# Kernel tuning notes

Hardware: AMD Instinct MI355X
Metric: run time of the kernel (lower is better)

## Reference

```python
import jax, jax.numpy as jnp
import numpy as np


def setup_inputs() -> dict:
    key = jax.random.key(0)
    k1, k2 = jax.random.split(key)
    query = jax.random.normal(k1, (1, 1024), dtype=jnp.float32)
    keys = jax.random.normal(k2, (32768, 1024), dtype=jnp.float32)
    return {"query": query, "keys": keys}


def reference(query, keys):
    # query: [1, H] -> squeeze to [H]; keys: [S, H]
    q = jnp.squeeze(query)                       # [H]
    dots = keys @ q                              # [S]
    q_norm = jnp.linalg.norm(q)                  # scalar
    k_norms = jnp.linalg.norm(keys, axis=-1)     # [S]
    cos_scores = dots / (q_norm * k_norms)       # [S] cosine similarity per key
    context = jnp.sum(cos_scores[:, None] * keys, axis=0)  # [H]
    return context[None, :]                      # [1, H]
```

## Files before the change

kernel.cpp:

```cpp
#include <hip/hip_runtime.h>


constexpr int H   = 1024;
constexpr int TPB = 256;
constexpr int WPB = TPB / 64;
constexpr int NBLOCKS = 512;
constexpr int R2_CHUNKS = 16;


template <bool USE_WS>
__global__ __launch_bounds__(TPB, 2)
void cosctx_main(const float* __restrict__ q,
                 const float* __restrict__ keys,
                 int S,
                 float* __restrict__ out,
                 float* __restrict__ ws)
{
    const int lane  = threadIdx.x & 63;
    const int wave  = threadIdx.x >> 6;
    const int gwave = blockIdx.x * WPB + wave;
    const int nwaves = gridDim.x * WPB;

    const float4* q4 = reinterpret_cast<const float4*>(q);
    const float4* k4 = reinterpret_cast<const float4*>(keys);

    float4 qv[4];
#pragma unroll
    for (int j = 0; j < 4; ++j) qv[j] = q4[j * 64 + lane];

    float qsq = 0.f;
#pragma unroll
    for (int j = 0; j < 4; ++j)
        qsq += qv[j].x * qv[j].x + qv[j].y * qv[j].y +
               qv[j].z * qv[j].z + qv[j].w * qv[j].w;
#pragma unroll
    for (int off = 32; off > 0; off >>= 1) qsq += __shfl_down(qsq, off, 64);
    const float inv_qn = rsqrtf(__shfl(qsq, 0, 64));

    float4 acc[4];
#pragma unroll
    for (int j = 0; j < 4; ++j) acc[j] = make_float4(0.f, 0.f, 0.f, 0.f);

    int row = gwave;
    float4 kv[4];
    if (row < S) {
        const float4* kr = k4 + (size_t)row * (H / 4);
#pragma unroll
        for (int j = 0; j < 4; ++j) kv[j] = kr[j * 64 + lane];
    }
    while (row < S) {
        const int nrow = row + nwaves;
        float4 kn[4];
        if (nrow < S) {
            const float4* kr = k4 + (size_t)nrow * (H / 4);
#pragma unroll
            for (int j = 0; j < 4; ++j) kn[j] = kr[j * 64 + lane];
        }

        float dot = 0.f, ksq = 0.f;
#pragma unroll
        for (int j = 0; j < 4; ++j) {
            dot += kv[j].x * qv[j].x + kv[j].y * qv[j].y +
                   kv[j].z * qv[j].z + kv[j].w * qv[j].w;
            ksq += kv[j].x * kv[j].x + kv[j].y * kv[j].y +
                   kv[j].z * kv[j].z + kv[j].w * kv[j].w;
        }
#pragma unroll
        for (int off = 32; off > 0; off >>= 1) {
            dot += __shfl_down(dot, off, 64);
            ksq += __shfl_down(ksq, off, 64);
        }
        const float score = __shfl(dot, 0, 64) * inv_qn *
                            rsqrtf(__shfl(ksq, 0, 64));

#pragma unroll
        for (int j = 0; j < 4; ++j) {
            acc[j].x += score * kv[j].x;
            acc[j].y += score * kv[j].y;
            acc[j].z += score * kv[j].z;
            acc[j].w += score * kv[j].w;
        }
#pragma unroll
        for (int j = 0; j < 4; ++j) kv[j] = kn[j];
        row = nrow;
    }

    __shared__ float sacc[WPB][H];
    float4* sa4 = reinterpret_cast<float4*>(sacc[wave]);
#pragma unroll
    for (int j = 0; j < 4; ++j) sa4[j * 64 + lane] = acc[j];
    __syncthreads();

    float4 v = make_float4(0.f, 0.f, 0.f, 0.f);
#pragma unroll
    for (int w = 0; w < WPB; ++w) {
        float4 u = reinterpret_cast<const float4*>(sacc[w])[threadIdx.x];
        v.x += u.x; v.y += u.y; v.z += u.z; v.w += u.w;
    }

    if (USE_WS) {
        reinterpret_cast<float4*>(ws)[(size_t)blockIdx.x * (H / 4) + threadIdx.x] = v;
    } else {
        const int c = threadIdx.x * 4;
        atomicAdd(out + c + 0, v.x);
        atomicAdd(out + c + 1, v.y);
        atomicAdd(out + c + 2, v.z);
        atomicAdd(out + c + 3, v.w);
    }
}

__global__ __launch_bounds__(256)
void cosctx_reduce(const float* __restrict__ ws, float* __restrict__ out)
{
    const int g  = blockIdx.x & 3;
    const int ch = blockIdx.x >> 2;
    const int c  = g * 256 + threadIdx.x;
    const int bpc = NBLOCKS / R2_CHUNKS;
    const int b0 = ch * bpc;
    float s = 0.f;
#pragma unroll 4
    for (int b = b0; b < b0 + bpc; ++b)
        s += ws[(size_t)b * H + c];
    atomicAdd(out + c, s);
}

extern "C" void kernel_launch(void* const* d_in, const int* in_sizes, int n_in,
                              void* d_out, int out_size, void* d_ws, size_t ws_size,
                              hipStream_t stream)
{
    const float* q    = (const float*)d_in[0];
    const float* keys = (const float*)d_in[1];
    float* out        = (float*)d_out;
    const int S = in_sizes[1] / H;

    hipMemsetAsync(out, 0, H * sizeof(float), stream);

    const size_t ws_need = (size_t)NBLOCKS * H * sizeof(float);
    if (ws_size >= ws_need) {
        cosctx_main<true><<<NBLOCKS, TPB, 0, stream>>>(q, keys, S, out, (float*)d_ws);
        cosctx_reduce<<<4 * R2_CHUNKS, 256, 0, stream>>>((const float*)d_ws, out);
    } else {
        cosctx_main<false><<<NBLOCKS, TPB, 0, stream>>>(q, keys, S, out, nullptr);
    }
}
```

Baseline: 195.8 us.

## Process two rows per iteration with deeper prefetch and atomic-free final reduction

The main loop now handles two key rows per iteration and prefetches the next two, which doubles the loads in flight per wave to better hide HBM latency. The second-stage reduction is rewritten so that each block fully reduces a 64-column slice across all partial blocks using float4 loads and shared memory, then writes the output directly. This removes the memset and the atomics on the workspace path. Holding more float4 registers may lower occupancy under launch_bounds(256,2).

```diff
diff --git a/kernel.cpp b/kernel.cpp
--- a/kernel.cpp
+++ b/kernel.cpp
@@ -5,7 +5,7 @@
 constexpr int TPB = 256;
 constexpr int WPB = TPB / 64;
 constexpr int NBLOCKS = 512;
-constexpr int R2_CHUNKS = 16;
+constexpr int RED_BLOCKS = H / 64;
 
 
 template <bool USE_WS>
@@ -19,7 +19,7 @@
     const int lane  = threadIdx.x & 63;
     const int wave  = threadIdx.x >> 6;
     const int gwave = blockIdx.x * WPB + wave;
-    const int nwaves = gridDim.x * WPB;
+    const int nw    = gridDim.x * WPB;
 
     const float4* q4 = reinterpret_cast<const float4*>(q);
     const float4* k4 = reinterpret_cast<const float4*>(keys);
@@ -41,48 +41,85 @@
 #pragma unroll
     for (int j = 0; j < 4; ++j) acc[j] = make_float4(0.f, 0.f, 0.f, 0.f);
 
-    int row = gwave;
-    float4 kv[4];
-    if (row < S) {
-        const float4* kr = k4 + (size_t)row * (H / 4);
+    int ra = gwave;
+    int rb = gwave + nw;
+    float4 ka[4], kb[4];
+    if (ra < S) {
+        const float4* kr = k4 + (size_t)ra * (H / 4);
 #pragma unroll
-        for (int j = 0; j < 4; ++j) kv[j] = kr[j * 64 + lane];
+        for (int j = 0; j < 4; ++j) ka[j] = kr[j * 64 + lane];
     }
-    while (row < S) {
-        const int nrow = row + nwaves;
-        float4 kn[4];
-        if (nrow < S) {
-            const float4* kr = k4 + (size_t)nrow * (H / 4);
+    if (rb < S) {
+        const float4* kr = k4 + (size_t)rb * (H / 4);
 #pragma unroll
-            for (int j = 0; j < 4; ++j) kn[j] = kr[j * 64 + lane];
+        for (int j = 0; j < 4; ++j) kb[j] = kr[j * 64 + lane];
+    }
+
+    while (ra < S) {
+        const int rc = ra + 2 * nw;
+        const int rd = rb + 2 * nw;
+        float4 kc[4], kd[4];
+        if (rc < S) {
+            const float4* kr = k4 + (size_t)rc * (H / 4);
+#pragma unroll
+            for (int j = 0; j < 4; ++j) kc[j] = kr[j * 64 + lane];
+        }
+        if (rd < S) {
+            const float4* kr = k4 + (size_t)rd * (H / 4);
+#pragma unroll
+            for (int j = 0; j < 4; ++j) kd[j] = kr[j * 64 + lane];
         }
 
-        float dot = 0.f, ksq = 0.f;
+        const bool hasB = (rb < S);
+
+        float dotA = 0.f, ksqA = 0.f, dotB = 0.f, ksqB = 0.f;
 #pragma unroll
         for (int j = 0; j < 4; ++j) {
-            dot += kv[j].x * qv[j].x + kv[j].y * qv[j].y +
-                   kv[j].z * qv[j].z + kv[j].w * qv[j].w;
-            ksq += kv[j].x * kv[j].x + kv[j].y * kv[j].y +
-                   kv[j].z * kv[j].z + kv[j].w * kv[j].w;
+            dotA += ka[j].x * qv[j].x + ka[j].y * qv[j].y +
+                    ka[j].z * qv[j].z + ka[j].w * qv[j].w;
+            ksqA += ka[j].x * ka[j].x + ka[j].y * ka[j].y +
+                    ka[j].z * ka[j].z + ka[j].w * ka[j].w;
+        }
+        if (hasB) {
+#pragma unroll
+            for (int j = 0; j < 4; ++j) {
+                dotB += kb[j].x * qv[j].x + kb[j].y * qv[j].y +
+                        kb[j].z * qv[j].z + kb[j].w * qv[j].w;
+                ksqB += kb[j].x * kb[j].x + kb[j].y * kb[j].y +
+                        kb[j].z * kb[j].z + kb[j].w * kb[j].w;
+            }
         }
 #pragma unroll
         for (int off = 32; off > 0; off >>= 1) {
-            dot += __shfl_down(dot, off, 64);
-            ksq += __shfl_down(ksq, off, 64);
+            dotA += __shfl_down(dotA, off, 64);
+            ksqA += __shfl_down(ksqA, off, 64);
+            dotB += __shfl_down(dotB, off, 64);
+            ksqB += __shfl_down(ksqB, off, 64);
         }
-        const float score = __shfl(dot, 0, 64) * inv_qn *
-                            rsqrtf(__shfl(ksq, 0, 64));
-
+        const float scoreA = __shfl(dotA, 0, 64) * inv_qn *
+                             rsqrtf(__shfl(ksqA, 0, 64));
 #pragma unroll
         for (int j = 0; j < 4; ++j) {
-            acc[j].x += score * kv[j].x;
-            acc[j].y += score * kv[j].y;
-            acc[j].z += score * kv[j].z;
-            acc[j].w += score * kv[j].w;
+            acc[j].x += scoreA * ka[j].x;
+            acc[j].y += scoreA * ka[j].y;
+            acc[j].z += scoreA * ka[j].z;
+            acc[j].w += scoreA * ka[j].w;
+        }
+        if (hasB) {
+            const float scoreB = __shfl(dotB, 0, 64) * inv_qn *
+                                 rsqrtf(__shfl(ksqB, 0, 64));
+#pragma unroll
+            for (int j = 0; j < 4; ++j) {
+                acc[j].x += scoreB * kb[j].x;
+                acc[j].y += scoreB * kb[j].y;
+                acc[j].z += scoreB * kb[j].z;
+                acc[j].w += scoreB * kb[j].w;
+            }
         }
 #pragma unroll
-        for (int j = 0; j < 4; ++j) kv[j] = kn[j];
-        row = nrow;
+        for (int j = 0; j < 4; ++j) { ka[j] = kc[j]; kb[j] = kd[j]; }
+        ra = rc;
+        rb = rd;
     }
 
     __shared__ float sacc[WPB][H];
@@ -112,16 +149,30 @@
 __global__ __launch_bounds__(256)
 void cosctx_reduce(const float* __restrict__ ws, float* __restrict__ out)
 {
-    const int g  = blockIdx.x & 3;
-    const int ch = blockIdx.x >> 2;
-    const int c  = g * 256 + threadIdx.x;
-    const int bpc = NBLOCKS / R2_CHUNKS;
-    const int b0 = ch * bpc;
-    float s = 0.f;
-#pragma unroll 4
-    for (int b = b0; b < b0 + bpc; ++b)
-        s += ws[(size_t)b * H + c];
-    atomicAdd(out + c, s);
+    const float4* w4 = reinterpret_cast<const float4*>(ws);
+    const int cq = threadIdx.x & 15;
+    const int rg = threadIdx.x >> 4;
+    const int base = blockIdx.x * 16 + cq;
+
+    float4 s = make_float4(0.f, 0.f, 0.f, 0.f);
+    for (int b = rg; b < NBLOCKS; b += 16) {
+        float4 u = w4[(size_t)b * (H / 4) + base];
+        s.x += u.x; s.y += u.y; s.z += u.z; s.w += u.w;
+    }
+
+    __shared__ float4 red[16][16];
+    red[rg][cq] = s;
+    __syncthreads();
+
+    if (threadIdx.x < 16) {
+        float4 r = red[0][threadIdx.x];
+#pragma unroll
+        for (int g = 1; g < 16; ++g) {
+            float4 u = red[g][threadIdx.x];
+            r.x += u.x; r.y += u.y; r.z += u.z; r.w += u.w;
+        }
+        reinterpret_cast<float4*>(out)[blockIdx.x * 16 + threadIdx.x] = r;
+    }
 }
 
 extern "C" void kernel_launch(void* const* d_in, const int* in_sizes, int n_in,
@@ -133,13 +184,12 @@
     float* out        = (float*)d_out;
     const int S = in_sizes[1] / H;
 
-    hipMemsetAsync(out, 0, H * sizeof(float), stream);
-
     const size_t ws_need = (size_t)NBLOCKS * H * sizeof(float);
     if (ws_size >= ws_need) {
         cosctx_main<true><<<NBLOCKS, TPB, 0, stream>>>(q, keys, S, out, (float*)d_ws);
-        cosctx_reduce<<<4 * R2_CHUNKS, 256, 0, stream>>>((const float*)d_ws, out);
+        cosctx_reduce<<<RED_BLOCKS, 256, 0, stream>>>((const float*)d_ws, out);
     } else {
+        hipMemsetAsync(out, 0, H * sizeof(float), stream);
         cosctx_main<false><<<NBLOCKS, TPB, 0, stream>>>(q, keys, S, out, nullptr);
     }
 }
```

Measured after the change: 202.0 us. 1.03x slower.
